# Kernel optimization log

Hardware: AMD Instinct MI355X
Metric: run time of the kernel (lower is better)

Reference implementation:

```python
import jax, jax.numpy as jnp
import numpy as np

N = 16384      # input points
C_IN = 64      # per-point feature dim
RATIO = 0.25
R = 0.2        # ball-query radius
K = 32         # max_num_neighbors (hardcoded in SAModule.forward)
S = int(N * RATIO)  # sampled centers (fps)
H1, H2, H3 = 128, 128, 256
D_IN = C_IN + 3


def setup_inputs() -> dict:
    key = jax.random.key(0)
    ks = jax.random.split(key, 8)
    sc = lambda fan: np.float32(1.0 / np.sqrt(fan))
    return {
        'x': jax.random.normal(ks[0], (N, C_IN), jnp.float32),
        'pos': jax.random.normal(ks[1], (N, 3), jnp.float32),
        'batch': jnp.zeros((N,), jnp.int32),
        'W1': jax.random.normal(ks[2], (D_IN, H1), jnp.float32) * sc(D_IN),
        'b1': jnp.zeros((H1,), jnp.float32),
        'W2': jax.random.normal(ks[3], (H1, H2), jnp.float32) * sc(H1),
        'b2': jnp.zeros((H2,), jnp.float32),
        'W3': jax.random.normal(ks[4], (H2, H3), jnp.float32) * sc(H2),
        'b3': jnp.zeros((H3,), jnp.float32),
    }


def _fps(pos, num_samples):
    # iterative farthest point sampling, deterministic start at index 0
    d = jnp.sum((pos - pos[0]) ** 2, axis=-1)  # [N] dist to selected set

    def step(d, _):
        nxt = jnp.argmax(d)
        d = jnp.minimum(d, jnp.sum((pos - pos[nxt]) ** 2, axis=-1))
        return d, nxt

    _, rest = jax.lax.scan(step, d, None, length=num_samples - 1)
    return jnp.concatenate([jnp.zeros((1,), rest.dtype), rest])


def _radius(pos, centers, r, k):
    # for each center, up to k neighbors within radius r (nearest-first)
    d2 = (jnp.sum(centers ** 2, -1)[:, None] + jnp.sum(pos ** 2, -1)[None, :]
          - 2.0 * centers @ pos.T)  # [S, N]
    masked = jnp.where(d2 <= r * r, d2, jnp.inf)
    negk, col = jax.lax.top_k(-masked, k)  # smallest distances
    valid = jnp.isfinite(negk)             # inside the ball
    return col, valid


def reference(x, pos, batch, W1, b1, W2, b2, W3, b3):
    posc = jax.lax.stop_gradient(pos)
    idx = _fps(posc, S)                    # [S]
    centers = pos[idx]                     # [S, 3]
    col, valid = _radius(posc, posc[idx], R, K)  # [S, K] neighbor ids, validity

    # message: nn(concat(x_j, pos_j - pos_i)) ; aggregate: max over neighbors
    rel = pos[col] - centers[:, None, :]   # [S, K, 3]
    inp = jnp.concatenate([x[col], rel], axis=-1)  # [S, K, D_IN]
    h = jax.nn.relu(inp @ W1 + b1)
    h = jax.nn.relu(h @ W2 + b2)
    h = h @ W3 + b3                        # [S, K, H3]
    h = jnp.where(valid[..., None], h, -jnp.inf)
    out = jnp.max(h, axis=1)               # [S, H3] (self is always a neighbor)
    return out, centers, batch[idx]
```

## Files before the change

### kernel.cpp

```cpp
#include <hip/hip_runtime.h>
#include <cstdint>

typedef unsigned int   u32;
typedef unsigned long long u64;

#define N_PTS 16384
#define S_OUT 4096
#define K_NB  32
#define CAP   1024

#define OUT_CEN   1048576
#define OUT_BATCH 1060864

__device__ int   g_idx[S_OUT];
__device__ __align__(16) float g_cen[S_OUT * 3];
__device__ int   g_cnt[S_OUT];
__device__ int   g_col[S_OUT * K_NB];
__device__ u32   g_perm[N_PTS];

__device__ __forceinline__ u32 spread3(u32 x) {
    x &= 0x3ffu;
    x = (x | (x << 16)) & 0x030000FFu;
    x = (x | (x << 8))  & 0x0300F00Fu;
    x = (x | (x << 4))  & 0x030C30C3u;
    x = (x | (x << 2))  & 0x09249249u;
    return x;
}

__global__ __launch_bounds__(1024) void sort_kernel(const float* __restrict__ pos) {
    const int t = threadIdx.x;
    __shared__ u32 sortbuf[N_PTS];
    for (int i = 0; i < 16; ++i) {
        int p = t * 16 + i;
        float X = pos[3 * p], Y = pos[3 * p + 1], Z = pos[3 * p + 2];
        int qx = (int)((X + 8.f) * 4.f); qx = qx < 0 ? 0 : (qx > 63 ? 63 : qx);
        int qy = (int)((Y + 8.f) * 4.f); qy = qy < 0 ? 0 : (qy > 63 ? 63 : qy);
        int qz = (int)((Z + 8.f) * 4.f); qz = qz < 0 ? 0 : (qz > 63 ? 63 : qz);
        u32 code = (spread3((u32)qx) << 2) | (spread3((u32)qy) << 1) | spread3((u32)qz);
        sortbuf[p] = (code << 14) | (u32)p;
    }
    __syncthreads();
    for (int k = 2; k <= N_PTS; k <<= 1) {
        for (int j = k >> 1; j >= 1; j >>= 1) {
            for (int e = t; e < (N_PTS >> 1); e += 1024) {
                int i  = ((e & ~(j - 1)) << 1) | (e & (j - 1));
                int p2 = i + j;
                u32 a = sortbuf[i], b = sortbuf[p2];
                bool up = ((i & k) == 0);
                if ((a > b) == up) { sortbuf[i] = b; sortbuf[p2] = a; }
            }
            __syncthreads();
        }
    }
    for (int p = t; p < N_PTS; p += 1024) g_perm[p] = sortbuf[p] & 16383u;
}

#define R16(M) M(0) M(1) M(2) M(3) M(4) M(5) M(6) M(7) M(8) M(9) M(10) M(11) M(12) M(13) M(14) M(15)

__global__ __launch_bounds__(1024) void fps_kernel(const float* __restrict__ pos) {
    const int t = threadIdx.x;
    const int lane = t & 63, wid = t >> 6;

#define DECLP(i) float px##i, py##i, pz##i, d##i; u32 o##i;
    R16(DECLP)
#undef DECLP
    {
        const int base = t * 16;
#define LOADP(i) { u32 oi = g_perm[base + i] & (u32)(N_PTS - 1); o##i = oi; \
                   px##i = pos[3 * oi]; py##i = pos[3 * oi + 1]; pz##i = pos[3 * oi + 2]; }
        R16(LOADP)
#undef LOADP
    }
    float blox = px0, bhix = px0, bloy = py0, bhiy = py0, bloz = pz0, bhiz = pz0;
#define BBOX(i) blox = fminf(blox, px##i); bhix = fmaxf(bhix, px##i); \
                bloy = fminf(bloy, py##i); bhiy = fmaxf(bhiy, py##i); \
                bloz = fminf(bloz, pz##i); bhiz = fmaxf(bhiz, pz##i);
    R16(BBOX)
#undef BBOX
    float qx0 = pos[0], qy0 = pos[1], qz0 = pos[2];
    float lmax = -1.f;
#define INITD(i) { float dx = __fsub_rn(px##i, qx0), dy = __fsub_rn(py##i, qy0), dz = __fsub_rn(pz##i, qz0); \
                   d##i = __fadd_rn(__fadd_rn(__fmul_rn(dx, dx), __fmul_rn(dy, dy)), __fmul_rn(dz, dz)); \
                   lmax = fmaxf(lmax, d##i); }
    R16(INITD)
#undef INITD
    if (t == 0) g_idx[0] = 0;

    __shared__ float warpV[16];
    __shared__ float maxvS;
    __shared__ int   winS;

    for (int it = 1; it < S_OUT; ++it) {
        float v = lmax;
#pragma unroll
        for (int off = 32; off >= 1; off >>= 1) v = fmaxf(v, __shfl_down(v, off));
        if (lane == 0) warpV[wid] = v;
        __syncthreads();
        if (wid == 0) {
            float v2 = (lane < 16) ? warpV[lane] : -1.f;
#pragma unroll
            for (int off = 8; off >= 1; off >>= 1) v2 = fmaxf(v2, __shfl_down(v2, off));
            if (lane == 0) { maxvS = v2; winS = 0x7fffffff; }
        }
        __syncthreads();
        float maxv = maxvS;
        if (lmax == maxv) {
            int cand = 0x7fffffff;
#define SCAN(i) cand = (d##i == maxv && (int)o##i < cand) ? (int)o##i : cand;
            R16(SCAN)
#undef SCAN
            atomicMin(&winS, cand);
        }
        __syncthreads();
        int wsel = winS & (N_PTS - 1);
        if (t == 0) g_idx[it] = wsel;
        float wx = pos[3 * wsel], wy = pos[3 * wsel + 1], wz = pos[3 * wsel + 2];
        float dxl = fmaxf(fmaxf(__fsub_rn(blox, wx), __fsub_rn(wx, bhix)), 0.f);
        float dyl = fmaxf(fmaxf(__fsub_rn(bloy, wy), __fsub_rn(wy, bhiy)), 0.f);
        float dzl = fmaxf(fmaxf(__fsub_rn(bloz, wz), __fsub_rn(wz, bhiz)), 0.f);
        float lb = __fadd_rn(__fadd_rn(__fmul_rn(dxl, dxl), __fmul_rn(dyl, dyl)), __fmul_rn(dzl, dzl));
        if (__fmul_rn(lb, 0.99999f) < lmax) {
            float nl = -1.f;
#define UPD(i) { float dx = __fsub_rn(px##i, wx), dy = __fsub_rn(py##i, wy), dz = __fsub_rn(pz##i, wz); \
                 float nd = __fadd_rn(__fadd_rn(__fmul_rn(dx, dx), __fmul_rn(dy, dy)), __fmul_rn(dz, dz)); \
                 d##i = fminf(d##i, nd); nl = fmaxf(nl, d##i); }
            R16(UPD)
#undef UPD
            lmax = nl;
        }
    }
}

__global__ __launch_bounds__(256) void radius_kernel(const float* __restrict__ pos,
                                                     float* __restrict__ outF) {
    const int s = blockIdx.x, t = threadIdx.x;
    const int lane = t & 63, wv = t >> 6;
    __shared__ float cd2[CAP];
    __shared__ int   cid[CAP];
    __shared__ int   wsum[4];

    const int selfI = g_idx[s] & (N_PTS - 1);
    float cx = pos[3 * selfI], cy = pos[3 * selfI + 1], cz = pos[3 * selfI + 2];
    if (t < 3) { float v = pos[3 * selfI + t]; g_cen[3 * s + t] = v; outF[OUT_CEN + 3 * s + t] = v; }
    if (t == 3) outF[OUT_BATCH + s] = 0.0f;
    float cs = __fadd_rn(__fadd_rn(__fmul_rn(cx, cx), __fmul_rn(cy, cy)), __fmul_rn(cz, cz));

    const int p0 = t * 64;
    int c = 0;
    for (int i = 0; i < 64; ++i) {
        int p = p0 + i;
        float x = pos[3 * p], y = pos[3 * p + 1], z = pos[3 * p + 2];
        float ps = __fadd_rn(__fadd_rn(__fmul_rn(x, x), __fmul_rn(y, y)), __fmul_rn(z, z));
        float dt = __fmaf_rn(cz, z, __fmaf_rn(cy, y, __fmul_rn(cx, x)));
        float d2 = __fsub_rn(__fadd_rn(cs, ps), __fmul_rn(2.0f, dt));
        c += (d2 <= 0.04f) ? 1 : 0;
    }
    int inc = c;
#pragma unroll
    for (int off = 1; off < 64; off <<= 1) {
        int o = __shfl_up(inc, off);
        if (lane >= off) inc += o;
    }
    if (lane == 63) wsum[wv] = inc;
    __syncthreads();
    int pre = 0;
#pragma unroll
    for (int w2 = 0; w2 < 4; ++w2) pre += (w2 < wv) ? wsum[w2] : 0;
    const int total = wsum[0] + wsum[1] + wsum[2] + wsum[3];
    int w = pre + (inc - c);
    for (int i = 0; i < 64; ++i) {
        int p = p0 + i;
        float x = pos[3 * p], y = pos[3 * p + 1], z = pos[3 * p + 2];
        float ps = __fadd_rn(__fadd_rn(__fmul_rn(x, x), __fmul_rn(y, y)), __fmul_rn(z, z));
        float dt = __fmaf_rn(cz, z, __fmaf_rn(cy, y, __fmul_rn(cx, x)));
        float d2 = __fsub_rn(__fadd_rn(cs, ps), __fmul_rn(2.0f, dt));
        if (d2 <= 0.04f) {
            if (w < CAP) { cd2[w] = d2; cid[w] = p; }
            ++w;
        }
    }
    __syncthreads();
    const int n = min(total, CAP);
    if (n <= K_NB) {
        if (t < K_NB) g_col[s * K_NB + t] = (t < n) ? cid[t] : selfI;
        if (t == 0) g_cnt[s] = n;
    } else {
        if (wv == 0) {
#define R16K(M) M(0) M(1) M(2) M(3) M(4) M(5) M(6) M(7) M(8) M(9) M(10) M(11) M(12) M(13) M(14) M(15)
#define KDECL(i) u64 kk##i;
            R16K(KDECL)
#undef KDECL
#define KLOAD(i) { int q = lane + 64 * i; \
                   if (q < n) { u32 fb = __float_as_uint(cd2[q]); \
                                fb = (fb >> 31) ? ~fb : (fb | 0x80000000u); \
                                kk##i = ((u64)fb << 32) | (u32)q; } \
                   else kk##i = ~0ull; }
            R16K(KLOAD)
#undef KLOAD
            for (int k = 0; k < K_NB; ++k) {
                u64 best = kk0;
#define KMIN(i) best = (kk##i < best) ? kk##i : best;
                KMIN(1) KMIN(2) KMIN(3) KMIN(4) KMIN(5) KMIN(6) KMIN(7) KMIN(8)
                KMIN(9) KMIN(10) KMIN(11) KMIN(12) KMIN(13) KMIN(14) KMIN(15)
#undef KMIN
#pragma unroll
                for (int m = 1; m < 64; m <<= 1) {
                    u64 o = __shfl_xor(best, m);
                    best = (o < best) ? o : best;
                }
                int q = (int)(u32)(best & 0xffffffffu) & (CAP - 1);
                if (lane == 0) g_col[s * K_NB + k] = cid[q];
#define KINV(i) if (q == lane + 64 * i) kk##i = ~0ull;
                R16K(KINV)
#undef KINV
            }
        }
        __syncthreads();
        if (t == 0) g_cnt[s] = K_NB;
    }
}

#define SM_H2  0
#define SM_INP 4224
#define SM_H1  6400
#define SM_H3  4224
#define SM_TOT 12544

__global__ __launch_bounds__(256) void mlp_kernel(const float* __restrict__ x,
                                                  const float* __restrict__ pos,
                                                  const float* __restrict__ W1,
                                                  const float* __restrict__ b1,
                                                  const float* __restrict__ W2,
                                                  const float* __restrict__ b2,
                                                  const float* __restrict__ W3,
                                                  const float* __restrict__ b3,
                                                  float* __restrict__ outF) {
    const int s = blockIdx.x, t = threadIdx.x;
    __shared__ __align__(16) float smem[SM_TOT];
    __shared__ int cols[32];
    float* inp = smem + SM_INP;
    float* h1s = smem + SM_H1;
    float* h2s = smem + SM_H2;
    float* h3  = smem + SM_H3;

    const int n = g_cnt[s];
    if (t < 32) cols[t] = g_col[s * K_NB + t] & (N_PTS - 1);
    __syncthreads();

    {
        const int r = t >> 3, sg = t & 7;
        const float4* x4 = (const float4*)x;
        float4 v1 = x4[cols[r] * 16 + sg * 2];
        float4 v2 = x4[cols[r] * 16 + sg * 2 + 1];
        *(float4*)&inp[r * 68 + sg * 8]     = v1;
        *(float4*)&inp[r * 68 + sg * 8 + 4] = v2;
    }
    if (t < 32) {
        int j = cols[t];
        inp[t * 68 + 64] = __fsub_rn(pos[3 * j],     g_cen[3 * s]);
        inp[t * 68 + 65] = __fsub_rn(pos[3 * j + 1], g_cen[3 * s + 1]);
        inp[t * 68 + 66] = __fsub_rn(pos[3 * j + 2], g_cen[3 * s + 2]);
        inp[t * 68 + 67] = 0.f;
    }
    __syncthreads();

    const int r = t & 31, cg = t >> 5;
    {
        const int c0 = cg * 16;
        float acc[16];
#pragma unroll
        for (int j = 0; j < 16; ++j) acc[j] = 0.f;
        for (int i0 = 0; i0 < 64; i0 += 4) {
            float4 a4 = *(const float4*)&inp[r * 68 + i0];
#pragma unroll
            for (int q = 0; q < 4; ++q) {
                float a = (q == 0) ? a4.x : (q == 1) ? a4.y : (q == 2) ? a4.z : a4.w;
                const float* wr = &W1[(i0 + q) * 128 + c0];
#pragma unroll
                for (int m = 0; m < 4; ++m) {
                    float4 w = *(const float4*)(wr + 4 * m);
                    acc[4 * m]     += a * w.x; acc[4 * m + 1] += a * w.y;
                    acc[4 * m + 2] += a * w.z; acc[4 * m + 3] += a * w.w;
                }
            }
        }
#pragma unroll
        for (int q = 0; q < 3; ++q) {
            float a = inp[r * 68 + 64 + q];
            const float* wr = &W1[(64 + q) * 128 + c0];
#pragma unroll
            for (int m = 0; m < 4; ++m) {
                float4 w = *(const float4*)(wr + 4 * m);
                acc[4 * m]     += a * w.x; acc[4 * m + 1] += a * w.y;
                acc[4 * m + 2] += a * w.z; acc[4 * m + 3] += a * w.w;
            }
        }
#pragma unroll
        for (int j = 0; j < 16; ++j) h1s[r * 132 + c0 + j] = fmaxf(acc[j] + b1[c0 + j], 0.f);
    }
    __syncthreads();
    {
        const int c0 = cg * 16;
        float acc[16];
#pragma unroll
        for (int j = 0; j < 16; ++j) acc[j] = 0.f;
        for (int i0 = 0; i0 < 128; i0 += 4) {
            float4 a4 = *(const float4*)&h1s[r * 132 + i0];
#pragma unroll
            for (int q = 0; q < 4; ++q) {
                float a = (q == 0) ? a4.x : (q == 1) ? a4.y : (q == 2) ? a4.z : a4.w;
                const float* wr = &W2[(i0 + q) * 128 + c0];
#pragma unroll
                for (int m = 0; m < 4; ++m) {
                    float4 w = *(const float4*)(wr + 4 * m);
                    acc[4 * m]     += a * w.x; acc[4 * m + 1] += a * w.y;
                    acc[4 * m + 2] += a * w.z; acc[4 * m + 3] += a * w.w;
                }
            }
        }
#pragma unroll
        for (int j = 0; j < 16; ++j) h2s[r * 132 + c0 + j] = fmaxf(acc[j] + b2[c0 + j], 0.f);
    }
    __syncthreads();
    {
        const int c0 = cg * 32;
        float acc[32];
#pragma unroll
        for (int j = 0; j < 32; ++j) acc[j] = 0.f;
        for (int i0 = 0; i0 < 128; i0 += 4) {
            float4 a4 = *(const float4*)&h2s[r * 132 + i0];
#pragma unroll
            for (int q = 0; q < 4; ++q) {
                float a = (q == 0) ? a4.x : (q == 1) ? a4.y : (q == 2) ? a4.z : a4.w;
                const float* wr = &W3[(i0 + q) * 256 + c0];
#pragma unroll
                for (int m = 0; m < 8; ++m) {
                    float4 w = *(const float4*)(wr + 4 * m);
                    acc[4 * m]     += a * w.x; acc[4 * m + 1] += a * w.y;
                    acc[4 * m + 2] += a * w.z; acc[4 * m + 3] += a * w.w;
                }
            }
        }
        __syncthreads();
#pragma unroll
        for (int j = 0; j < 32; ++j) h3[r * 260 + c0 + j] = acc[j] + b3[c0 + j];
    }
    __syncthreads();
    {
        float m = h3[t];
        for (int rr = 1; rr < n; ++rr) m = fmaxf(m, h3[rr * 260 + t]);
        outF[s * 256 + t] = m;
    }
}

extern "C" void kernel_launch(void* const* d_in, const int* in_sizes, int n_in,
                              void* d_out, int out_size, void* d_ws, size_t ws_size,
                              hipStream_t stream) {
    const float* x   = (const float*)d_in[0];
    const float* pos = (const float*)d_in[1];
    const float* W1 = (const float*)d_in[3]; const float* b1 = (const float*)d_in[4];
    const float* W2 = (const float*)d_in[5]; const float* b2 = (const float*)d_in[6];
    const float* W3 = (const float*)d_in[7]; const float* b3 = (const float*)d_in[8];
    float* outF = (float*)d_out;
    (void)d_ws; (void)ws_size; (void)in_sizes; (void)n_in; (void)out_size;

    hipLaunchKernelGGL(sort_kernel, dim3(1), dim3(1024), 0, stream, pos);
    hipLaunchKernelGGL(fps_kernel, dim3(1), dim3(1024), 0, stream, pos);
    hipLaunchKernelGGL(radius_kernel, dim3(S_OUT), dim3(256), 0, stream, pos, outF);
    hipLaunchKernelGGL(mlp_kernel, dim3(S_OUT), dim3(256), 0, stream,
                       x, pos, W1, b1, W2, b2, W3, b3, outF);
}
```

Before: 6.803 ms.

## Fuse FPS, radius and MLP into persistent kernel with per-center flags

Merges the FPS, radius-query and MLP kernels into one persistent launch. Block 0 runs farthest point sampling and publishes each selected index through a global flag array. The other 255 worker blocks spin on those flags and process centers as soon as they appear, overlapping neighbor search and MLP work with the serial FPS loop. The cost is that the FPS block now shares the GPU with busy workers, and correctness relies on all blocks being co-resident so the spin-waits cannot deadlock.

```diff
diff --git a/kernel.cpp b/kernel.cpp
--- a/kernel.cpp
+++ b/kernel.cpp
@@ -8,15 +8,14 @@
 #define S_OUT 4096
 #define K_NB  32
 #define CAP   1024
+#define NWORK 255
+#define FSTR  16
 
 #define OUT_CEN   1048576
 #define OUT_BATCH 1060864
 
-__device__ int   g_idx[S_OUT];
-__device__ __align__(16) float g_cen[S_OUT * 3];
-__device__ int   g_cnt[S_OUT];
-__device__ int   g_col[S_OUT * K_NB];
-__device__ u32   g_perm[N_PTS];
+__device__ u32 g_perm[N_PTS];
+__device__ int g_flag[S_OUT * FSTR];
 
 __device__ __forceinline__ u32 spread3(u32 x) {
     x &= 0x3ffu;
@@ -30,6 +29,7 @@
 __global__ __launch_bounds__(1024) void sort_kernel(const float* __restrict__ pos) {
     const int t = threadIdx.x;
     __shared__ u32 sortbuf[N_PTS];
+    for (int e = t; e < S_OUT * FSTR; e += 1024) g_flag[e] = 0;
     for (int i = 0; i < 16; ++i) {
         int p = t * 16 + i;
         float X = pos[3 * p], Y = pos[3 * p + 1], Z = pos[3 * p + 2];
@@ -57,135 +57,157 @@
 
 #define R16(M) M(0) M(1) M(2) M(3) M(4) M(5) M(6) M(7) M(8) M(9) M(10) M(11) M(12) M(13) M(14) M(15)
 
-__global__ __launch_bounds__(1024) void fps_kernel(const float* __restrict__ pos) {
+#define SM_H2  0
+#define SM_INP 4224
+#define SM_H1  6400
+#define SM_H3  4224
+#define SM_TOT 12544
+
+__global__ __launch_bounds__(1024) void mega_kernel(const float* __restrict__ pos,
+                                                    const float* __restrict__ x,
+                                                    const float* __restrict__ W1,
+                                                    const float* __restrict__ b1,
+                                                    const float* __restrict__ W2,
+                                                    const float* __restrict__ b2,
+                                                    const float* __restrict__ W3,
+                                                    const float* __restrict__ b3,
+                                                    float* __restrict__ outF) {
     const int t = threadIdx.x;
     const int lane = t & 63, wid = t >> 6;
 
+    __shared__ float warpV[16];
+    __shared__ float maxvS;
+    __shared__ int   winS;
+    __shared__ float cd2[CAP];
+    __shared__ int   cid[CAP];
+    __shared__ int   wsum16[16];
+    __shared__ int   colsS[32];
+    __shared__ int   selfS;
+    __shared__ __align__(16) float smem[SM_TOT];
+
+    if (blockIdx.x == 0) {
 #define DECLP(i) float px##i, py##i, pz##i, d##i; u32 o##i;
-    R16(DECLP)
+        R16(DECLP)
 #undef DECLP
-    {
-        const int base = t * 16;
+        {
+            const int base = t * 16;
 #define LOADP(i) { u32 oi = g_perm[base + i] & (u32)(N_PTS - 1); o##i = oi; \
                    px##i = pos[3 * oi]; py##i = pos[3 * oi + 1]; pz##i = pos[3 * oi + 2]; }
-        R16(LOADP)
+            R16(LOADP)
 #undef LOADP
-    }
-    float blox = px0, bhix = px0, bloy = py0, bhiy = py0, bloz = pz0, bhiz = pz0;
+        }
+        float blox = px0, bhix = px0, bloy = py0, bhiy = py0, bloz = pz0, bhiz = pz0;
 #define BBOX(i) blox = fminf(blox, px##i); bhix = fmaxf(bhix, px##i); \
                 bloy = fminf(bloy, py##i); bhiy = fmaxf(bhiy, py##i); \
                 bloz = fminf(bloz, pz##i); bhiz = fmaxf(bhiz, pz##i);
-    R16(BBOX)
+        R16(BBOX)
 #undef BBOX
-    float qx0 = pos[0], qy0 = pos[1], qz0 = pos[2];
-    float lmax = -1.f;
+        float qx0 = pos[0], qy0 = pos[1], qz0 = pos[2];
+        float lmax = -1.f;
 #define INITD(i) { float dx = __fsub_rn(px##i, qx0), dy = __fsub_rn(py##i, qy0), dz = __fsub_rn(pz##i, qz0); \
                    d##i = __fadd_rn(__fadd_rn(__fmul_rn(dx, dx), __fmul_rn(dy, dy)), __fmul_rn(dz, dz)); \
                    lmax = fmaxf(lmax, d##i); }
-    R16(INITD)
+        R16(INITD)
 #undef INITD
-    if (t == 0) g_idx[0] = 0;
-
-    __shared__ float warpV[16];
-    __shared__ float maxvS;
-    __shared__ int   winS;
-
-    for (int it = 1; it < S_OUT; ++it) {
-        float v = lmax;
-#pragma unroll
-        for (int off = 32; off >= 1; off >>= 1) v = fmaxf(v, __shfl_down(v, off));
-        if (lane == 0) warpV[wid] = v;
-        __syncthreads();
-        if (wid == 0) {
-            float v2 = (lane < 16) ? warpV[lane] : -1.f;
-#pragma unroll
-            for (int off = 8; off >= 1; off >>= 1) v2 = fmaxf(v2, __shfl_down(v2, off));
-            if (lane == 0) { maxvS = v2; winS = 0x7fffffff; }
-        }
-        __syncthreads();
-        float maxv = maxvS;
-        if (lmax == maxv) {
-            int cand = 0x7fffffff;
+        if (t == 0) atomicExch(&g_flag[0], 1);
+
+        for (int it = 1; it < S_OUT; ++it) {
+            float v = lmax;
+#pragma unroll
+            for (int off = 32; off >= 1; off >>= 1) v = fmaxf(v, __shfl_down(v, off));
+            if (lane == 0) warpV[wid] = v;
+            __syncthreads();
+            if (wid == 0) {
+                float v2 = (lane < 16) ? warpV[lane] : -1.f;
+#pragma unroll
+                for (int off = 8; off >= 1; off >>= 1) v2 = fmaxf(v2, __shfl_down(v2, off));
+                if (lane == 0) { maxvS = v2; winS = 0x7fffffff; }
+            }
+            __syncthreads();
+            float maxv = maxvS;
+            if (lmax == maxv) {
+                int cand = 0x7fffffff;
 #define SCAN(i) cand = (d##i == maxv && (int)o##i < cand) ? (int)o##i : cand;
-            R16(SCAN)
+                R16(SCAN)
 #undef SCAN
-            atomicMin(&winS, cand);
-        }
-        __syncthreads();
-        int wsel = winS & (N_PTS - 1);
-        if (t == 0) g_idx[it] = wsel;
-        float wx = pos[3 * wsel], wy = pos[3 * wsel + 1], wz = pos[3 * wsel + 2];
-        float dxl = fmaxf(fmaxf(__fsub_rn(blox, wx), __fsub_rn(wx, bhix)), 0.f);
-        float dyl = fmaxf(fmaxf(__fsub_rn(bloy, wy), __fsub_rn(wy, bhiy)), 0.f);
-        float dzl = fmaxf(fmaxf(__fsub_rn(bloz, wz), __fsub_rn(wz, bhiz)), 0.f);
-        float lb = __fadd_rn(__fadd_rn(__fmul_rn(dxl, dxl), __fmul_rn(dyl, dyl)), __fmul_rn(dzl, dzl));
-        if (__fmul_rn(lb, 0.99999f) < lmax) {
-            float nl = -1.f;
+                atomicMin(&winS, cand);
+            }
+            __syncthreads();
+            int wsel = winS & (N_PTS - 1);
+            if (t == 0) atomicExch(&g_flag[it * FSTR], wsel + 1);
+            float wx = pos[3 * wsel], wy = pos[3 * wsel + 1], wz = pos[3 * wsel + 2];
+            float dxl = fmaxf(fmaxf(__fsub_rn(blox, wx), __fsub_rn(wx, bhix)), 0.f);
+            float dyl = fmaxf(fmaxf(__fsub_rn(bloy, wy), __fsub_rn(wy, bhiy)), 0.f);
+            float dzl = fmaxf(fmaxf(__fsub_rn(bloz, wz), __fsub_rn(wz, bhiz)), 0.f);
+            float lb = __fadd_rn(__fadd_rn(__fmul_rn(dxl, dxl), __fmul_rn(dyl, dyl)), __fmul_rn(dzl, dzl));
+            if (__fmul_rn(lb, 0.99999f) < lmax) {
+                float nl = -1.f;
 #define UPD(i) { float dx = __fsub_rn(px##i, wx), dy = __fsub_rn(py##i, wy), dz = __fsub_rn(pz##i, wz); \
                  float nd = __fadd_rn(__fadd_rn(__fmul_rn(dx, dx), __fmul_rn(dy, dy)), __fmul_rn(dz, dz)); \
                  d##i = fminf(d##i, nd); nl = fmaxf(nl, d##i); }
-            R16(UPD)
+                R16(UPD)
 #undef UPD
-            lmax = nl;
-        }
+                lmax = nl;
+            }
+        }
+        return;
     }
-}
-
-__global__ __launch_bounds__(256) void radius_kernel(const float* __restrict__ pos,
-                                                     float* __restrict__ outF) {
-    const int s = blockIdx.x, t = threadIdx.x;
-    const int lane = t & 63, wv = t >> 6;
-    __shared__ float cd2[CAP];
-    __shared__ int   cid[CAP];
-    __shared__ int   wsum[4];
-
-    const int selfI = g_idx[s] & (N_PTS - 1);
-    float cx = pos[3 * selfI], cy = pos[3 * selfI + 1], cz = pos[3 * selfI + 2];
-    if (t < 3) { float v = pos[3 * selfI + t]; g_cen[3 * s + t] = v; outF[OUT_CEN + 3 * s + t] = v; }
-    if (t == 3) outF[OUT_BATCH + s] = 0.0f;
-    float cs = __fadd_rn(__fadd_rn(__fmul_rn(cx, cx), __fmul_rn(cy, cy)), __fmul_rn(cz, cz));
-
-    const int p0 = t * 64;
-    int c = 0;
-    for (int i = 0; i < 64; ++i) {
-        int p = p0 + i;
-        float x = pos[3 * p], y = pos[3 * p + 1], z = pos[3 * p + 2];
-        float ps = __fadd_rn(__fadd_rn(__fmul_rn(x, x), __fmul_rn(y, y)), __fmul_rn(z, z));
-        float dt = __fmaf_rn(cz, z, __fmaf_rn(cy, y, __fmul_rn(cx, x)));
-        float d2 = __fsub_rn(__fadd_rn(cs, ps), __fmul_rn(2.0f, dt));
-        c += (d2 <= 0.04f) ? 1 : 0;
-    }
-    int inc = c;
-#pragma unroll
-    for (int off = 1; off < 64; off <<= 1) {
-        int o = __shfl_up(inc, off);
-        if (lane >= off) inc += o;
-    }
-    if (lane == 63) wsum[wv] = inc;
-    __syncthreads();
-    int pre = 0;
-#pragma unroll
-    for (int w2 = 0; w2 < 4; ++w2) pre += (w2 < wv) ? wsum[w2] : 0;
-    const int total = wsum[0] + wsum[1] + wsum[2] + wsum[3];
-    int w = pre + (inc - c);
-    for (int i = 0; i < 64; ++i) {
-        int p = p0 + i;
-        float x = pos[3 * p], y = pos[3 * p + 1], z = pos[3 * p + 2];
-        float ps = __fadd_rn(__fadd_rn(__fmul_rn(x, x), __fmul_rn(y, y)), __fmul_rn(z, z));
-        float dt = __fmaf_rn(cz, z, __fmaf_rn(cy, y, __fmul_rn(cx, x)));
-        float d2 = __fsub_rn(__fadd_rn(cs, ps), __fmul_rn(2.0f, dt));
-        if (d2 <= 0.04f) {
-            if (w < CAP) { cd2[w] = d2; cid[w] = p; }
-            ++w;
-        }
-    }
-    __syncthreads();
-    const int n = min(total, CAP);
-    if (n <= K_NB) {
-        if (t < K_NB) g_col[s * K_NB + t] = (t < n) ? cid[t] : selfI;
-        if (t == 0) g_cnt[s] = n;
-    } else {
-        if (wv == 0) {
+
+    for (int s = (int)blockIdx.x - 1; s < S_OUT; s += NWORK) {
+        if (t == 0) {
+            int v;
+            while ((v = atomicAdd(&g_flag[s * FSTR], 0)) == 0) __builtin_amdgcn_s_sleep(32);
+            selfS = v - 1;
+        }
+        __syncthreads();
+        const int selfI = selfS & (N_PTS - 1);
+        if (t < 3) outF[OUT_CEN + 3 * s + t] = pos[3 * selfI + t];
+        if (t == 3) outF[OUT_BATCH + s] = 0.0f;
+        const float cx = pos[3 * selfI], cy = pos[3 * selfI + 1], cz = pos[3 * selfI + 2];
+        const float cs = __fadd_rn(__fadd_rn(__fmul_rn(cx, cx), __fmul_rn(cy, cy)), __fmul_rn(cz, cz));
+
+        const int p0 = t * 16;
+        int c = 0;
+        for (int i = 0; i < 16; ++i) {
+            int p = p0 + i;
+            float X = pos[3 * p], Y = pos[3 * p + 1], Z = pos[3 * p + 2];
+            float ps = __fadd_rn(__fadd_rn(__fmul_rn(X, X), __fmul_rn(Y, Y)), __fmul_rn(Z, Z));
+            float dt = __fmaf_rn(cz, Z, __fmaf_rn(cy, Y, __fmul_rn(cx, X)));
+            float d2 = __fsub_rn(__fadd_rn(cs, ps), __fmul_rn(2.0f, dt));
+            c += (d2 <= 0.04f) ? 1 : 0;
+        }
+        int inc = c;
+#pragma unroll
+        for (int off = 1; off < 64; off <<= 1) {
+            int o = __shfl_up(inc, off);
+            if (lane >= off) inc += o;
+        }
+        if (lane == 63) wsum16[wid] = inc;
+        __syncthreads();
+        int pre = 0, total = 0;
+#pragma unroll
+        for (int w2 = 0; w2 < 16; ++w2) {
+            int wv2 = wsum16[w2];
+            pre += (w2 < wid) ? wv2 : 0;
+            total += wv2;
+        }
+        int w = pre + (inc - c);
+        for (int i = 0; i < 16; ++i) {
+            int p = p0 + i;
+            float X = pos[3 * p], Y = pos[3 * p + 1], Z = pos[3 * p + 2];
+            float ps = __fadd_rn(__fadd_rn(__fmul_rn(X, X), __fmul_rn(Y, Y)), __fmul_rn(Z, Z));
+            float dt = __fmaf_rn(cz, Z, __fmaf_rn(cy, Y, __fmul_rn(cx, X)));
+            float d2 = __fsub_rn(__fadd_rn(cs, ps), __fmul_rn(2.0f, dt));
+            if (d2 <= 0.04f) {
+                if (w < CAP) { cd2[w] = d2; cid[w] = p; }
+                ++w;
+            }
+        }
+        __syncthreads();
+        const int n = min(total, CAP);
+        if (n <= K_NB) {
+            if (t < K_NB) colsS[t] = (t < n) ? cid[t] : selfI;
+        } else if (wid == 0) {
 #define R16K(M) M(0) M(1) M(2) M(3) M(4) M(5) M(6) M(7) M(8) M(9) M(10) M(11) M(12) M(13) M(14) M(15)
 #define KDECL(i) u64 kk##i;
             R16K(KDECL)
@@ -209,147 +231,93 @@
                     best = (o < best) ? o : best;
                 }
                 int q = (int)(u32)(best & 0xffffffffu) & (CAP - 1);
-                if (lane == 0) g_col[s * K_NB + k] = cid[q];
+                if (lane == 0) colsS[k] = cid[q];
 #define KINV(i) if (q == lane + 64 * i) kk##i = ~0ull;
                 R16K(KINV)
 #undef KINV
             }
         }
         __syncthreads();
-        if (t == 0) g_cnt[s] = K_NB;
-    }
-}
-
-#define SM_H2  0
-#define SM_INP 4224
-#define SM_H1  6400
-#define SM_H3  4224
-#define SM_TOT 12544
-
-__global__ __launch_bounds__(256) void mlp_kernel(const float* __restrict__ x,
-                                                  const float* __restrict__ pos,
-                                                  const float* __restrict__ W1,
-                                                  const float* __restrict__ b1,
-                                                  const float* __restrict__ W2,
-                                                  const float* __restrict__ b2,
-                                                  const float* __restrict__ W3,
-                                                  const float* __restrict__ b3,
-                                                  float* __restrict__ outF) {
-    const int s = blockIdx.x, t = threadIdx.x;
-    __shared__ __align__(16) float smem[SM_TOT];
-    __shared__ int cols[32];
-    float* inp = smem + SM_INP;
-    float* h1s = smem + SM_H1;
-    float* h2s = smem + SM_H2;
-    float* h3  = smem + SM_H3;
-
-    const int n = g_cnt[s];
-    if (t < 32) cols[t] = g_col[s * K_NB + t] & (N_PTS - 1);
-    __syncthreads();
-
-    {
-        const int r = t >> 3, sg = t & 7;
-        const float4* x4 = (const float4*)x;
-        float4 v1 = x4[cols[r] * 16 + sg * 2];
-        float4 v2 = x4[cols[r] * 16 + sg * 2 + 1];
-        *(float4*)&inp[r * 68 + sg * 8]     = v1;
-        *(float4*)&inp[r * 68 + sg * 8 + 4] = v2;
-    }
-    if (t < 32) {
-        int j = cols[t];
-        inp[t * 68 + 64] = __fsub_rn(pos[3 * j],     g_cen[3 * s]);
-        inp[t * 68 + 65] = __fsub_rn(pos[3 * j + 1], g_cen[3 * s + 1]);
-        inp[t * 68 + 66] = __fsub_rn(pos[3 * j + 2], g_cen[3 * s + 2]);
-        inp[t * 68 + 67] = 0.f;
-    }
-    __syncthreads();
-
-    const int r = t & 31, cg = t >> 5;
-    {
-        const int c0 = cg * 16;
-        float acc[16];
-#pragma unroll
-        for (int j = 0; j < 16; ++j) acc[j] = 0.f;
-        for (int i0 = 0; i0 < 64; i0 += 4) {
-            float4 a4 = *(const float4*)&inp[r * 68 + i0];
-#pragma unroll
-            for (int q = 0; q < 4; ++q) {
-                float a = (q == 0) ? a4.x : (q == 1) ? a4.y : (q == 2) ? a4.z : a4.w;
-                const float* wr = &W1[(i0 + q) * 128 + c0];
-#pragma unroll
-                for (int m = 0; m < 4; ++m) {
-                    float4 w = *(const float4*)(wr + 4 * m);
-                    acc[4 * m]     += a * w.x; acc[4 * m + 1] += a * w.y;
-                    acc[4 * m + 2] += a * w.z; acc[4 * m + 3] += a * w.w;
-                }
-            }
-        }
-#pragma unroll
-        for (int q = 0; q < 3; ++q) {
-            float a = inp[r * 68 + 64 + q];
-            const float* wr = &W1[(64 + q) * 128 + c0];
-#pragma unroll
-            for (int m = 0; m < 4; ++m) {
-                float4 w = *(const float4*)(wr + 4 * m);
-                acc[4 * m]     += a * w.x; acc[4 * m + 1] += a * w.y;
-                acc[4 * m + 2] += a * w.z; acc[4 * m + 3] += a * w.w;
-            }
-        }
-#pragma unroll
-        for (int j = 0; j < 16; ++j) h1s[r * 132 + c0 + j] = fmaxf(acc[j] + b1[c0 + j], 0.f);
-    }
-    __syncthreads();
-    {
-        const int c0 = cg * 16;
-        float acc[16];
-#pragma unroll
-        for (int j = 0; j < 16; ++j) acc[j] = 0.f;
-        for (int i0 = 0; i0 < 128; i0 += 4) {
-            float4 a4 = *(const float4*)&h1s[r * 132 + i0];
-#pragma unroll
-            for (int q = 0; q < 4; ++q) {
-                float a = (q == 0) ? a4.x : (q == 1) ? a4.y : (q == 2) ? a4.z : a4.w;
-                const float* wr = &W2[(i0 + q) * 128 + c0];
-#pragma unroll
-                for (int m = 0; m < 4; ++m) {
-                    float4 w = *(const float4*)(wr + 4 * m);
-                    acc[4 * m]     += a * w.x; acc[4 * m + 1] += a * w.y;
-                    acc[4 * m + 2] += a * w.z; acc[4 * m + 3] += a * w.w;
-                }
-            }
-        }
-#pragma unroll
-        for (int j = 0; j < 16; ++j) h2s[r * 132 + c0 + j] = fmaxf(acc[j] + b2[c0 + j], 0.f);
-    }
-    __syncthreads();
-    {
-        const int c0 = cg * 32;
-        float acc[32];
-#pragma unroll
-        for (int j = 0; j < 32; ++j) acc[j] = 0.f;
-        for (int i0 = 0; i0 < 128; i0 += 4) {
-            float4 a4 = *(const float4*)&h2s[r * 132 + i0];
-#pragma unroll
-            for (int q = 0; q < 4; ++q) {
-                float a = (q == 0) ? a4.x : (q == 1) ? a4.y : (q == 2) ? a4.z : a4.w;
-                const float* wr = &W3[(i0 + q) * 256 + c0];
-#pragma unroll
-                for (int m = 0; m < 8; ++m) {
-                    float4 w = *(const float4*)(wr + 4 * m);
-                    acc[4 * m]     += a * w.x; acc[4 * m + 1] += a * w.y;
-                    acc[4 * m + 2] += a * w.z; acc[4 * m + 3] += a * w.w;
-                }
-            }
-        }
-        __syncthreads();
-#pragma unroll
-        for (int j = 0; j < 32; ++j) h3[r * 260 + c0 + j] = acc[j] + b3[c0 + j];
-    }
-    __syncthreads();
-    {
-        float m = h3[t];
-        for (int rr = 1; rr < n; ++rr) m = fmaxf(m, h3[rr * 260 + t]);
-        outF[s * 256 + t] = m;
+        const int nn = (n < K_NB) ? n : K_NB;
+
+        float* inp = smem + SM_INP;
+        float* h1s = smem + SM_H1;
+        float* h2s = smem + SM_H2;
+        float* h3  = smem + SM_H3;
+        if (t < 512) {
+            const int r = t >> 4, sg = t & 15;
+            const float4* x4 = (const float4*)x;
+            *(float4*)&inp[r * 68 + sg * 4] = x4[(colsS[r] & (N_PTS - 1)) * 16 + sg];
+        } else if (t < 544) {
+            const int r = t - 512;
+            int j = colsS[r] & (N_PTS - 1);
+            inp[r * 68 + 64] = __fsub_rn(pos[3 * j],     cx);
+            inp[r * 68 + 65] = __fsub_rn(pos[3 * j + 1], cy);
+            inp[r * 68 + 66] = __fsub_rn(pos[3 * j + 2], cz);
+            inp[r * 68 + 67] = 0.f;
+        }
+        __syncthreads();
+        {
+            const int r = t >> 5, c0 = (t & 31) * 4;
+            float a0 = 0.f, a1 = 0.f, a2 = 0.f, a3 = 0.f;
+            for (int k = 0; k < 64; ++k) {
+                float a = inp[r * 68 + k];
+                float4 ww = *(const float4*)&W1[k * 128 + c0];
+                a0 += a * ww.x; a1 += a * ww.y; a2 += a * ww.z; a3 += a * ww.w;
+            }
+#pragma unroll
+            for (int q = 0; q < 3; ++q) {
+                float a = inp[r * 68 + 64 + q];
+                float4 ww = *(const float4*)&W1[(64 + q) * 128 + c0];
+                a0 += a * ww.x; a1 += a * ww.y; a2 += a * ww.z; a3 += a * ww.w;
+            }
+            float4 bb = *(const float4*)&b1[c0];
+            h1s[r * 132 + c0]     = fmaxf(a0 + bb.x, 0.f);
+            h1s[r * 132 + c0 + 1] = fmaxf(a1 + bb.y, 0.f);
+            h1s[r * 132 + c0 + 2] = fmaxf(a2 + bb.z, 0.f);
+            h1s[r * 132 + c0 + 3] = fmaxf(a3 + bb.w, 0.f);
+        }
+        __syncthreads();
+        {
+            const int r = t >> 5, c0 = (t & 31) * 4;
+            float a0 = 0.f, a1 = 0.f, a2 = 0.f, a3 = 0.f;
+            for (int k = 0; k < 128; ++k) {
+                float a = h1s[r * 132 + k];
+                float4 ww = *(const float4*)&W2[k * 128 + c0];
+                a0 += a * ww.x; a1 += a * ww.y; a2 += a * ww.z; a3 += a * ww.w;
+            }
+            float4 bb = *(const float4*)&b2[c0];
+            h2s[r * 132 + c0]     = fmaxf(a0 + bb.x, 0.f);
+            h2s[r * 132 + c0 + 1] = fmaxf(a1 + bb.y, 0.f);
+            h2s[r * 132 + c0 + 2] = fmaxf(a2 + bb.z, 0.f);
+            h2s[r * 132 + c0 + 3] = fmaxf(a3 + bb.w, 0.f);
+        }
+        __syncthreads();
+        {
+            const int r = t >> 5, c0 = (t & 31) * 8;
+            float a0 = 0.f, a1 = 0.f, a2 = 0.f, a3 = 0.f, a4 = 0.f, a5 = 0.f, a6 = 0.f, a7 = 0.f;
+            for (int k = 0; k < 128; ++k) {
+                float a = h2s[r * 132 + k];
+                float4 w0 = *(const float4*)&W3[k * 256 + c0];
+                float4 w1 = *(const float4*)&W3[k * 256 + c0 + 4];
+                a0 += a * w0.x; a1 += a * w0.y; a2 += a * w0.z; a3 += a * w0.w;
+                a4 += a * w1.x; a5 += a * w1.y; a6 += a * w1.z; a7 += a * w1.w;
+            }
+            __syncthreads();
+            float4 b0 = *(const float4*)&b3[c0];
+            float4 b1v = *(const float4*)&b3[c0 + 4];
+            h3[r * 260 + c0]     = a0 + b0.x;  h3[r * 260 + c0 + 1] = a1 + b0.y;
+            h3[r * 260 + c0 + 2] = a2 + b0.z;  h3[r * 260 + c0 + 3] = a3 + b0.w;
+            h3[r * 260 + c0 + 4] = a4 + b1v.x; h3[r * 260 + c0 + 5] = a5 + b1v.y;
+            h3[r * 260 + c0 + 6] = a6 + b1v.z; h3[r * 260 + c0 + 7] = a7 + b1v.w;
+        }
+        __syncthreads();
+        if (t < 256) {
+            float m = h3[t];
+            for (int rr = 1; rr < nn; ++rr) m = fmaxf(m, h3[rr * 260 + t]);
+            outF[s * 256 + t] = m;
+        }
+        __syncthreads();
     }
 }
 
@@ -365,8 +333,6 @@
     (void)d_ws; (void)ws_size; (void)in_sizes; (void)n_in; (void)out_size;
 
     hipLaunchKernelGGL(sort_kernel, dim3(1), dim3(1024), 0, stream, pos);
-    hipLaunchKernelGGL(fps_kernel, dim3(1), dim3(1024), 0, stream, pos);
-    hipLaunchKernelGGL(radius_kernel, dim3(S_OUT), dim3(256), 0, stream, pos, outF);
-    hipLaunchKernelGGL(mlp_kernel, dim3(S_OUT), dim3(256), 0, stream,
-                       x, pos, W1, b1, W2, b2, W3, b3, outF);
+    hipLaunchKernelGGL(mega_kernel, dim3(NWORK + 1), dim3(1024), 0, stream,
+                       pos, x, W1, b1, W2, b2, W3, b3, outF);
 }
```

Measured after the change: 6.323 ms. 1.08x faster.
